# Optimization experiments

Measured on AMD Instinct MI355X. Metric: run time of the kernel, lower is better.

Reference implementation:

```python
import jax, jax.numpy as jnp
import numpy as np

EPS = 1e-6

def rms_norm(x):
    # RMSNorm, affine=False
    return x * jax.lax.rsqrt(jnp.mean(x * x, axis=-1, keepdims=True) + EPS)

def apply_rope(x, cos, sin):
    # x: [N, T, h, d], cos/sin: [T, d//2], half-split rotation
    x1, x2 = jnp.split(x, 2, axis=-1)
    c = cos[None, :, None, :]
    s = sin[None, :, None, :]
    return jnp.concatenate([x1 * c - x2 * s, x1 * s + x2 * c], axis=-1)

def setup_inputs() -> dict:
    key = jax.random.key(0)
    k0, k1, k2 = jax.random.split(key, 3)
    N, T, D, hd = 1, 2048, 2048, 128
    input_NTD = jax.random.normal(k0, (N, T, D), jnp.float32)
    qkv_weight = jax.random.normal(k1, (3, D, D), jnp.float32) / np.sqrt(D) / 2.0
    o_weight = jax.random.normal(k2, (D, D), jnp.float32) * 0.02
    # standard 1d RoPE angle table
    pos = jnp.arange(T, dtype=jnp.float32)
    inv_freq = 1.0 / (10000.0 ** (jnp.arange(hd // 2, dtype=jnp.float32) / (hd // 2)))
    ang = pos[:, None] * inv_freq[None, :]  # [T, hd//2]
    return {
        "input_NTD": input_NTD,
        "qkv_weight": qkv_weight,
        "o_weight": o_weight,
        "cos": jnp.cos(ang),
        "sin": jnp.sin(ang),
    }

def reference(input_NTD, qkv_weight, o_weight, cos, sin):
    N, T, D = input_NTD.shape
    hd = cos.shape[-1] * 2
    h = D // hd
    w = qkv_weight.reshape(3 * D, D)
    qkv = rms_norm(input_NTD) @ w.T                      # [N, T, 3D]
    qkv = qkv.reshape(N, T, 3 * h, hd)
    q, k, v = jnp.split(qkv, 3, axis=2)                  # each [N, T, h, hd]
    q = apply_rope(rms_norm(q), cos, sin)
    k = apply_rope(rms_norm(k), cos, sin)
    scale = 1.0 / np.sqrt(hd)
    scores = jnp.einsum('nqhd,nkhd->nhqk', q, k) * scale  # [N, h, T, T]
    causal = jnp.tril(jnp.ones((T, T), bool))
    scores = jnp.where(causal[None, None], scores, -jnp.inf)
    att = jax.nn.softmax(scores, axis=-1)
    x = jnp.einsum('nhqk,nkhd->nqhd', att, v).reshape(N, T, D)
    out = input_NTD + x @ o_weight.T
    return out, k, v
```

## Files before the change

kernel.cpp:

```cpp
#include <hip/hip_runtime.h>
#include <hip/hip_bf16.h>

typedef unsigned short u16;
typedef unsigned int u32;
typedef __bf16 bf16x8 __attribute__((ext_vector_type(8)));
typedef u16 u16x8 __attribute__((ext_vector_type(8)));
typedef u16 u16x4 __attribute__((ext_vector_type(4)));
typedef float f32x4 __attribute__((ext_vector_type(4)));

#define T_SEQ 2048
#define DMODEL 2048
#define NHEAD 16
#define HDIM 128
#define ATT_SCALE 0.08838834764831843f

__device__ __forceinline__ u16 f2bf(float f) {
    return __builtin_bit_cast(u16, __float2bfloat16(f));
}
__device__ __forceinline__ bf16x8 as_bf(u16x8 v) {
    return __builtin_bit_cast(bf16x8, v);
}
__device__ __forceinline__ float lo2f(u32 w) { return __builtin_bit_cast(float, w << 16); }
__device__ __forceinline__ float hi2f(u32 w) { return __builtin_bit_cast(float, w & 0xffff0000u); }
__device__ __forceinline__ void gload_lds16(const u16* g, u16* l) {
    __builtin_amdgcn_global_load_lds(
        (const __attribute__((address_space(1))) u32*)(g),
        (__attribute__((address_space(3))) u32*)(l), 16, 0, 0);
}

__global__ __launch_bounds__(256) void prep(const float* __restrict__ w1,
                                            const float* __restrict__ w2,
                                            const float* __restrict__ x,
                                            u16* __restrict__ d1,
                                            u16* __restrict__ d2,
                                            u16* __restrict__ xn) {
    const int b = blockIdx.x, tid = threadIdx.x;
    if (b < 8192) {
        int i = b * 256 + tid;
        const float* src; u16* dst; int k;
        if (i < 1572864) { src = w1; dst = d1; k = i; }
        else             { src = w2; dst = d2; k = i - 1572864; }
        float4 a = ((const float4*)src)[2 * k];
        float4 bb = ((const float4*)src)[2 * k + 1];
        u16x8 o;
        o[0] = f2bf(a.x); o[1] = f2bf(a.y); o[2] = f2bf(a.z); o[3] = f2bf(a.w);
        o[4] = f2bf(bb.x); o[5] = f2bf(bb.y); o[6] = f2bf(bb.z); o[7] = f2bf(bb.w);
        *(u16x8*)(dst + (size_t)k * 8) = o;
        return;
    }
    const int row = b - 8192;
    const float* xr = x + (size_t)row * DMODEL;
    float4 a = ((const float4*)xr)[2 * tid];
    float4 bb = ((const float4*)xr)[2 * tid + 1];
    float ss = a.x*a.x + a.y*a.y + a.z*a.z + a.w*a.w
             + bb.x*bb.x + bb.y*bb.y + bb.z*bb.z + bb.w*bb.w;
#pragma unroll
    for (int off = 32; off; off >>= 1) ss += __shfl_xor(ss, off);
    __shared__ float red[4];
    if ((tid & 63) == 0) red[tid >> 6] = ss;
    __syncthreads();
    float tot = red[0] + red[1] + red[2] + red[3];
    float r = rsqrtf(tot * (1.f / DMODEL) + 1e-6f);
    u16x8 o;
    o[0] = f2bf(a.x*r); o[1] = f2bf(a.y*r); o[2] = f2bf(a.z*r); o[3] = f2bf(a.w*r);
    o[4] = f2bf(bb.x*r); o[5] = f2bf(bb.y*r); o[6] = f2bf(bb.z*r); o[7] = f2bf(bb.w*r);
    *(u16x8*)(xn + (size_t)row * DMODEL + tid * 8) = o;
}

#define VM2 asm volatile("s_waitcnt vmcnt(2)" ::: "memory");
#define VM4 asm volatile("s_waitcnt vmcnt(4)" ::: "memory");
#define VM0 asm volatile("s_waitcnt vmcnt(0)" ::: "memory");

#define ENDP                                                                  \
  __builtin_amdgcn_s_barrier();                                               \
  __builtin_amdgcn_sched_barrier(0);

#define LDA192(BUF, MH)                                                       \
  _Pragma("unroll") for (int mq = 0; mq < 4; ++mq) {                          \
    int ra = wr + (MH) * 64 + mq * 16 + fr;                                   \
    int sw = ra & 7;                                                          \
    _Pragma("unroll") for (int k2 = 0; k2 < 2; ++k2)                          \
      av[mq][k2] = *(const u16x8*)(sA[BUF] + ra * 64 +                        \
                                   ((((k2 << 2) | fg) ^ sw) << 3));           \
  }

#define LDB0_192(BUF)                                                         \
  _Pragma("unroll") for (int nq = 0; nq < 2; ++nq) {                          \
    int rb = wc + nq * 16 + fr;                                               \
    int sw = rb & 7;                                                          \
    _Pragma("unroll") for (int k2 = 0; k2 < 2; ++k2)                          \
      bv[nq][k2] = *(const u16x8*)(sB[BUF] + rb * 64 +                        \
                                   ((((k2 << 2) | fg) ^ sw) << 3));           \
  }

#define LDB1_192(BUF)                                                         \
  {                                                                           \
    int rb = wc + 32 + fr;                                                    \
    int sw = rb & 7;                                                          \
    _Pragma("unroll") for (int k2 = 0; k2 < 2; ++k2)                          \
      bv1[k2] = *(const u16x8*)(sB[BUF] + rb * 64 +                           \
                                ((((k2 << 2) | fg) ^ sw) << 3));              \
  }

#define MFMAQ_N0(MH)                                                          \
  __builtin_amdgcn_s_barrier();                                               \
  __builtin_amdgcn_s_setprio(1);                                              \
  _Pragma("unroll") for (int k2 = 0; k2 < 2; ++k2)                            \
    _Pragma("unroll") for (int mq = 0; mq < 4; ++mq)                          \
      _Pragma("unroll") for (int nq = 0; nq < 2; ++nq)                        \
        acc[(MH) * 4 + mq][nq] = __builtin_amdgcn_mfma_f32_16x16x32_bf16(     \
            as_bf(av[mq][k2]), as_bf(bv[nq][k2]), acc[(MH) * 4 + mq][nq],     \
            0, 0, 0);                                                         \
  __builtin_amdgcn_s_setprio(0);

#define MFMAQ_N1(MH)                                                          \
  __builtin_amdgcn_s_barrier();                                               \
  __builtin_amdgcn_s_setprio(1);                                              \
  _Pragma("unroll") for (int k2 = 0; k2 < 2; ++k2)                            \
    _Pragma("unroll") for (int mq = 0; mq < 4; ++mq)                          \
      acc[(MH) * 4 + mq][2] = __builtin_amdgcn_mfma_f32_16x16x32_bf16(        \
          as_bf(av[mq][k2]), as_bf(bv1[k2]), acc[(MH) * 4 + mq][2],           \
          0, 0, 0);                                                           \
  __builtin_amdgcn_s_setprio(0);

__global__ __launch_bounds__(512) void gemm192(const u16* __restrict__ A,
                                               const u16* __restrict__ B,
                                               u16* __restrict__ C,
                                               int M, int N, int K) {
    extern __shared__ char smem[];
    const int tid = threadIdx.x, lane = tid & 63, wid = tid >> 6;
    const int bm = blockIdx.y * 256, bn = blockIdx.x * 192;
    const int wr = (wid >> 2) * 128, wc = (wid & 3) * 48;
    const int fr = lane & 15, fg = lane >> 4;

    u16* sA[2] = {(u16*)smem, (u16*)(smem + 57344)};
    u16* sB[2] = {(u16*)(smem + 32768), (u16*)(smem + 90112)};

    const int cs = (((tid & 7) ^ ((tid >> 3) & 7)) << 3);
    const int s8 = (tid & 7) << 3;
    const int rr6 = tid >> 3;

    auto stA = [&](int buf, int k0, int mh) {
#pragma unroll
        for (int j = 0; j < 2; ++j) {
            int r = j * 128 + mh * 64 + rr6;
            gload_lds16(A + (size_t)(bm + r) * K + k0 + cs, sA[buf] + r * 64 + s8);
        }
    };
    auto stB = [&](int buf, int k0, int bt) {
        int r = bt * 64 + rr6;
        gload_lds16(B + (size_t)(bn + r) * K + k0 + cs, sB[buf] + r * 64 + s8);
    };

    f32x4 acc[8][3] = {};
    u16x8 av[4][2], bv[2][2], bv1[2];
    const int nt = K >> 6;

    stA(0, 0, 0); stA(0, 0, 1); stB(0, 0, 0); stB(0, 0, 1); stB(0, 0, 2);
    stA(1, 64, 0);
    VM2
    __builtin_amdgcn_s_barrier();
    __builtin_amdgcn_sched_barrier(0);

    for (int it = 0; it < (nt >> 1); ++it) {
        const int kc = it << 7;
        const int kn1 = kc + 64, kn2 = kc + 128, kn3 = kc + 192;
        const bool st2 = (kn2 < K), st3 = (kn3 < K);

        LDA192(0, 0) LDB0_192(0)
        stA(1, kn1, 1); stB(1, kn1, 0);
        MFMAQ_N0(0) ENDP
        LDB1_192(0)
        stB(1, kn1, 1); stB(1, kn1, 2);
        MFMAQ_N1(0) ENDP
        LDA192(0, 1)
        if (st2) stA(0, kn2, 0);
        MFMAQ_N1(1) ENDP
        LDB0_192(0)
        MFMAQ_N0(1)
        if (st2) { VM2 } else { VM0 }
        ENDP
        LDA192(1, 0) LDB0_192(1)
        if (st2) { stA(0, kn2, 1); stB(0, kn2, 0); }
        MFMAQ_N0(0) ENDP
        LDB1_192(1)
        if (st2) { stB(0, kn2, 1); stB(0, kn2, 2); }
        MFMAQ_N1(0) ENDP
        LDA192(1, 1)
        if (st3) stA(1, kn3, 0);
        MFMAQ_N1(1) ENDP
        LDB0_192(1)
        MFMAQ_N0(1)
        if (st3) { VM2 } else { VM0 }
        ENDP
    }

#pragma unroll
    for (int am = 0; am < 8; ++am)
#pragma unroll
        for (int bq = 0; bq < 3; ++bq)
#pragma unroll
            for (int r = 0; r < 4; ++r) {
                int row = bm + wr + am * 16 + fg * 4 + r;
                int col = bn + wc + bq * 16 + fr;
                C[(size_t)row * N + col] = f2bf(acc[am][bq][r]);
            }
}

#define LDAH(BUF, MH)                                                         \
  _Pragma("unroll") for (int mq = 0; mq < 2; ++mq) {                          \
    int ra = wr + (MH) * 32 + mq * 16 + fr;                                   \
    int sw = ra & 7;                                                          \
    _Pragma("unroll") for (int k2 = 0; k2 < 2; ++k2)                          \
      av[mq][k2] = *(const u16x8*)(sA[BUF] + ra * 64 +                        \
                                   ((((k2 << 2) | fg) ^ sw) << 3));           \
  }

#define LDBH(BUF, NH)                                                         \
  _Pragma("unroll") for (int nq = 0; nq < 2; ++nq) {                          \
    int rb = wc + (NH) * 32 + nq * 16 + fr;                                   \
    int sw = rb & 7;                                                          \
    _Pragma("unroll") for (int k2 = 0; k2 < 2; ++k2)                          \
      bv[nq][k2] = *(const u16x8*)(sB[BUF] + rb * 64 +                        \
                                   ((((k2 << 2) | fg) ^ sw) << 3));           \
  }

#define MFMAQH(MH, NH)                                                        \
  __builtin_amdgcn_s_barrier();                                               \
  __builtin_amdgcn_s_setprio(1);                                              \
  _Pragma("unroll") for (int k2 = 0; k2 < 2; ++k2)                            \
    _Pragma("unroll") for (int mq = 0; mq < 2; ++mq)                          \
      _Pragma("unroll") for (int nq = 0; nq < 2; ++nq)                        \
        acc[(MH) * 2 + mq][(NH) * 2 + nq] =                                   \
            __builtin_amdgcn_mfma_f32_16x16x32_bf16(                          \
                as_bf(av[mq][k2]), as_bf(bv[nq][k2]),                         \
                acc[(MH) * 2 + mq][(NH) * 2 + nq], 0, 0, 0);                  \
  __builtin_amdgcn_s_setprio(0);

__global__ __launch_bounds__(256) void gemm128(const u16* __restrict__ A,
                                               const u16* __restrict__ B,
                                               float* __restrict__ C,
                                               const float* __restrict__ resid,
                                               int M, int N, int K) {
    extern __shared__ char smem[];
    const int tid = threadIdx.x, lane = tid & 63, wid = tid >> 6;
    const int bm = blockIdx.y * 128, bn = blockIdx.x * 128;
    const int wr = (wid >> 1) * 64, wc = (wid & 1) * 64;
    const int fr = lane & 15, fg = lane >> 4;

    u16* sA[2] = {(u16*)smem, (u16*)(smem + 32768)};
    u16* sB[2] = {(u16*)(smem + 16384), (u16*)(smem + 49152)};

    const int cs = (((tid & 7) ^ ((tid >> 3) & 7)) << 3);
    const int s8 = (tid & 7) << 3;
    const int rr5 = tid >> 3;

    auto stA = [&](int buf, int k0, int mh) {
#pragma unroll
        for (int j = 0; j < 2; ++j) {
            int r = j * 64 + mh * 32 + rr5;
            gload_lds16(A + (size_t)(bm + r) * K + k0 + cs, sA[buf] + r * 64 + s8);
        }
    };
    auto stB = [&](int buf, int k0, int nh) {
#pragma unroll
        for (int j = 0; j < 2; ++j) {
            int r = j * 64 + nh * 32 + rr5;
            gload_lds16(B + (size_t)(bn + r) * K + k0 + cs, sB[buf] + r * 64 + s8);
        }
    };

    f32x4 acc[4][4] = {};
    u16x8 av[2][2], bv[2][2];
    const int nt = K >> 6;

    stA(0, 0, 0); stA(0, 0, 1); stB(0, 0, 0); stB(0, 0, 1);
    stA(1, 64, 0); stB(1, 64, 1);
    VM4
    __builtin_amdgcn_s_barrier();
    __builtin_amdgcn_sched_barrier(0);

    for (int it = 0; it < (nt >> 1); ++it) {
        const int kc = it << 7;
        const int kn1 = kc + 64, kn2 = kc + 128, kn3 = kc + 192;
        const bool st2 = (kn2 < K), st3 = (kn3 < K);

        LDAH(0, 0) LDBH(0, 0)
        stA(1, kn1, 1);
        MFMAQH(0, 0) ENDP
        LDBH(0, 1)
        stB(1, kn1, 0);
        MFMAQH(0, 1) ENDP
        LDAH(0, 1)
        if (st2) stA(0, kn2, 0);
        MFMAQH(1, 1) ENDP
        LDBH(0, 0)
        if (st2) stB(0, kn2, 1);
        MFMAQH(1, 0)
        if (st2) { VM4 } else { VM0 }
        ENDP
        LDAH(1, 0) LDBH(1, 0)
        if (st2) stA(0, kn2, 1);
        MFMAQH(0, 0) ENDP
        LDBH(1, 1)
        if (st2) stB(0, kn2, 0);
        MFMAQH(0, 1) ENDP
        LDAH(1, 1)
        if (st3) stA(1, kn3, 0);
        MFMAQH(1, 1) ENDP
        LDBH(1, 0)
        if (st3) stB(1, kn3, 1);
        MFMAQH(1, 0)
        VM4
        ENDP
    }

#pragma unroll
    for (int am = 0; am < 4; ++am)
#pragma unroll
        for (int bq = 0; bq < 4; ++bq)
#pragma unroll
            for (int r = 0; r < 4; ++r) {
                int row = bm + wr + am * 16 + fg * 4 + r;
                int col = bn + wc + bq * 16 + fr;
                float val = acc[am][bq][r] + resid[(size_t)row * N + col];
                C[(size_t)row * N + col] = val;
            }
}

__global__ __launch_bounds__(256) void rope_split(const u16* __restrict__ qkv,
                                                  const float* __restrict__ cosb,
                                                  const float* __restrict__ sinb,
                                                  u16* __restrict__ q_bf,
                                                  u16* __restrict__ k_bf,
                                                  float* __restrict__ k_out,
                                                  float* __restrict__ v_out) {
    const int t = blockIdx.x, tid = threadIdx.x, wid = tid >> 6, lane = tid & 63;
    const u16* row = qkv + (size_t)t * (3 * DMODEL);
    const int dp = (lane & 31) << 1;
    float2 c2 = *(const float2*)(cosb + t * 64 + dp);
    float2 s2 = *(const float2*)(sinb + t * 64 + dp);
    const bool hi = lane >= 32;

    for (int task = wid; task < 32; task += 4) {
        u32 w = *(const u32*)(row + task * 128 + lane * 2);
        float xa = lo2f(w), xb = hi2f(w);
        float ss = xa * xa + xb * xb;
#pragma unroll
        for (int off = 32; off; off >>= 1) ss += __shfl_xor(ss, off);
        float rn = rsqrtf(ss * (1.f / 128.f) + 1e-6f);
        float pa = __shfl_xor(xa, 32), pb = __shfl_xor(xb, 32);
        float oa, ob;
        if (!hi) {
            oa = (xa * c2.x - pa * s2.x) * rn;
            ob = (xb * c2.y - pb * s2.y) * rn;
        } else {
            oa = (pa * s2.x + xa * c2.x) * rn;
            ob = (pb * s2.y + xb * c2.y) * rn;
        }
        u32 pk = (u32)f2bf(oa) | ((u32)f2bf(ob) << 16);
        if (task < 16) {
            *(u32*)(q_bf + ((size_t)task * T_SEQ + t) * 128 + lane * 2) = pk;
        } else {
            int hh = task - 16;
            *(u32*)(k_bf + ((size_t)hh * T_SEQ + t) * 128 + lane * 2) = pk;
            float2 kk; kk.x = oa; kk.y = ob;
            *(float2*)(k_out + (size_t)t * DMODEL + hh * 128 + lane * 2) = kk;
        }
    }
    {
        u16x8 vv = *(const u16x8*)(row + 2 * DMODEL + tid * 8);
        float4 f0, f1;
        f0.x = __builtin_bit_cast(float, (u32)vv[0] << 16);
        f0.y = __builtin_bit_cast(float, (u32)vv[1] << 16);
        f0.z = __builtin_bit_cast(float, (u32)vv[2] << 16);
        f0.w = __builtin_bit_cast(float, (u32)vv[3] << 16);
        f1.x = __builtin_bit_cast(float, (u32)vv[4] << 16);
        f1.y = __builtin_bit_cast(float, (u32)vv[5] << 16);
        f1.z = __builtin_bit_cast(float, (u32)vv[6] << 16);
        f1.w = __builtin_bit_cast(float, (u32)vv[7] << 16);
        *(float4*)(v_out + (size_t)t * DMODEL + tid * 8) = f0;
        *(float4*)(v_out + (size_t)t * DMODEL + tid * 8 + 4) = f1;
    }
}

__global__ __launch_bounds__(256) void vtrans(const u16* __restrict__ qkv,
                                              u16* __restrict__ vt) {
    const int b = blockIdx.x, tid = threadIdx.x;
    const int head = b >> 7;
    const int i = (b & 127) * 256 + tid;
    const int d = i & 127, tc = i >> 7;
    u16x8 o;
#pragma unroll
    for (int j = 0; j < 8; ++j)
        o[j] = qkv[(size_t)(tc * 8 + j) * (3 * DMODEL) + 2 * DMODEL + head * 128 + d];
    *(u16x8*)&vt[((size_t)head * 128 + d) * T_SEQ + tc * 8] = o;
}

__global__ __launch_bounds__(256) void attn_fwd(const u16* __restrict__ qb,
                                                const u16* __restrict__ kb,
                                                const u16* __restrict__ vtb,
                                                u16* __restrict__ xout) {
    __shared__ u16 Ks[2][64 * 128];
    __shared__ u16 Vs[2][128 * 64];
    __shared__ u16 Ps[4][16 * 64];

    const int bid = blockIdx.x;
    const int r8 = bid & 7, s = bid >> 3;
    const int head = r8 + ((s >> 5) << 3);
    const int j = s & 31;
    const int qt = (s < 32) ? (31 - j) : j;

    const int tid = threadIdx.x, wid = tid >> 6, lane = tid & 63;
    const int fr = lane & 15, fg = lane >> 4;
    const u16* kh = kb + (size_t)head * T_SEQ * 128;
    const u16* vth = vtb + (size_t)head * 128 * T_SEQ;
    const u16* qh = qb + (size_t)head * T_SEQ * 128;
    const int q0 = qt * 64 + wid * 16;
    const int qrow_g = q0 + fr;

    u16x8 bq[4];
    {
        const u16* qrow = qh + (size_t)(q0 + fr) * 128 + fg * 8;
#pragma unroll
        for (int cc = 0; cc < 4; ++cc) bq[cc] = *(const u16x8*)(qrow + cc * 32);
    }

    auto stage = [&](int kv0, int buf) {
#pragma unroll
        for (int i = 0; i < 4; ++i) {
            int idx = i * 256 + tid;
            int r = idx >> 4;
            int cbs = ((idx & 15) << 4) ^ ((r & 7) << 4);
            gload_lds16(kh + (size_t)(kv0 + r) * 128 + (cbs >> 1), &Ks[buf][idx * 8]);
        }
#pragma unroll
        for (int i = 0; i < 4; ++i) {
            int idx = i * 256 + tid;
            int d = idx >> 3;
            int cbs = ((idx & 7) << 4) ^ ((d & 7) << 4);
            gload_lds16(vth + (size_t)d * T_SEQ + kv0 + (cbs >> 1), &Vs[buf][idx * 8]);
        }
    };

    stage(0, 0);

    f32x4 o[8] = {};
    float m_run = -1e30f, l_run = 0.f;
    const int nt = qt + 1;

    for (int kt = 0; kt < nt; ++kt) {
        const int kv0 = kt * 64;
        const int buf = kt & 1;
        if (kt + 1 < nt) {
            stage(kv0 + 64, buf ^ 1);
            asm volatile("s_waitcnt vmcnt(8)" ::: "memory");
        } else {
            asm volatile("s_waitcnt vmcnt(0)" ::: "memory");
        }
        __builtin_amdgcn_s_barrier();
        __builtin_amdgcn_sched_barrier(0);

        const char* ksb = (const char*)&Ks[buf][0];
        const char* vsb = (const char*)&Vs[buf][0];
        char* psb = (char*)&Ps[wid][0];

        float p[4][4];
        float mx = -1e30f;
        const bool diag = (kv0 + 64 > q0);
#pragma unroll
        for (int st = 0; st < 4; ++st) {
            f32x4 sacc = {0.f, 0.f, 0.f, 0.f};
#pragma unroll
            for (int c4 = 0; c4 < 4; ++c4) {
                int r = st * 16 + fr;
                int cb = c4 * 64 + fg * 16;
                u16x8 ak = *(const u16x8*)(ksb + r * 256 + (cb ^ ((r & 7) << 4)));
                sacc = __builtin_amdgcn_mfma_f32_16x16x32_bf16(
                    as_bf(ak), as_bf(bq[c4]), sacc, 0, 0, 0);
            }
#pragma unroll
            for (int rr = 0; rr < 4; ++rr) {
                float sv = sacc[rr] * ATT_SCALE;
                if (diag) {
                    int kvg = kv0 + st * 16 + fg * 4 + rr;
                    sv = (kvg <= qrow_g) ? sv : -1e30f;
                }
                p[st][rr] = sv;
                mx = fmaxf(mx, sv);
            }
        }
        mx = fmaxf(mx, __shfl_xor(mx, 16));
        mx = fmaxf(mx, __shfl_xor(mx, 32));

        if (__all(mx - m_run <= 8.f)) {
            float rs = 0.f;
#pragma unroll
            for (int st = 0; st < 4; ++st) {
                u16x4 pw;
#pragma unroll
                for (int rr = 0; rr < 4; ++rr) {
                    float e = __expf(p[st][rr] - m_run);
                    rs += e;
                    pw[rr] = f2bf(e);
                }
                *(u16x4*)(psb + fr * 128 + ((st * 32 + fg * 8) ^ ((fr & 7) << 4))) = pw;
            }
            rs += __shfl_xor(rs, 16);
            rs += __shfl_xor(rs, 32);
            l_run += rs;
        } else {
            float m_new = fmaxf(m_run, mx);
            float corr = __expf(m_run - m_new);
            float rs = 0.f;
#pragma unroll
            for (int st = 0; st < 4; ++st) {
                u16x4 pw;
#pragma unroll
                for (int rr = 0; rr < 4; ++rr) {
                    float e = __expf(p[st][rr] - m_new);
                    rs += e;
                    pw[rr] = f2bf(e);
                }
                *(u16x4*)(psb + fr * 128 + ((st * 32 + fg * 8) ^ ((fr & 7) << 4))) = pw;
            }
            rs += __shfl_xor(rs, 16);
            rs += __shfl_xor(rs, 32);
            l_run = l_run * corr + rs;
            m_run = m_new;
            float ct[4];
#pragma unroll
            for (int rr = 0; rr < 4; ++rr) ct[rr] = __shfl(corr, fg * 4 + rr);
#pragma unroll
            for (int f = 0; f < 8; ++f)
#pragma unroll
                for (int rr = 0; rr < 4; ++rr) o[f][rr] *= ct[rr];
        }

#pragma unroll
        for (int ks = 0; ks < 2; ++ks) {
            u16x8 pa = *(const u16x8*)(psb + fr * 128 + ((ks * 64 + fg * 16) ^ ((fr & 7) << 4)));
#pragma unroll
            for (int f = 0; f < 8; ++f) {
                int d = f * 16 + fr;
                u16x8 vB = *(const u16x8*)(vsb + d * 128 + ((ks * 64 + fg * 16) ^ ((d & 7) << 4)));
                o[f] = __builtin_amdgcn_mfma_f32_16x16x32_bf16(
                    as_bf(pa), as_bf(vB), o[f], 0, 0, 0);
            }
        }
        __builtin_amdgcn_s_barrier();
    }

    float li[4];
#pragma unroll
    for (int rr = 0; rr < 4; ++rr) li[rr] = __shfl(l_run, fg * 4 + rr);
#pragma unroll
    for (int f = 0; f < 8; ++f)
#pragma unroll
        for (int rr = 0; rr < 4; ++rr) {
            int trow = q0 + fg * 4 + rr;
            float val = o[f][rr] / li[rr];
            xout[(size_t)trow * DMODEL + head * 128 + f * 16 + fr] = f2bf(val);
        }
}

extern "C" void kernel_launch(void* const* d_in, const int* in_sizes, int n_in,
                              void* d_out, int out_size, void* d_ws, size_t ws_size,
                              hipStream_t stream) {
    const float* x_in = (const float*)d_in[0];
    const float* w_qkv = (const float*)d_in[1];
    const float* w_o = (const float*)d_in[2];
    const float* cosb = (const float*)d_in[3];
    const float* sinb = (const float*)d_in[4];

    float* out = (float*)d_out;
    float* k_out = out + 4194304;
    float* v_out = out + 8388608;

    char* ws = (char*)d_ws;
    u16* xn    = (u16*)(ws);
    u16* w_bf  = (u16*)(ws + (size_t)(8u << 20));
    u16* o_bf  = (u16*)(ws + (size_t)(32u << 20));
    u16* qkv   = (u16*)(ws + (size_t)(40u << 20));
    u16* q_bf  = (u16*)(ws + (size_t)(64u << 20));
    u16* k_bf  = (u16*)(ws + (size_t)(72u << 20));
    u16* vt_bf = (u16*)(ws + (size_t)(80u << 20));
    u16* x_bf  = (u16*)(ws + (size_t)(88u << 20));

    (void)hipFuncSetAttribute(reinterpret_cast<const void*>(&gemm192),
                              hipFuncAttributeMaxDynamicSharedMemorySize, 114688);
    (void)hipFuncSetAttribute(reinterpret_cast<const void*>(&gemm128),
                              hipFuncAttributeMaxDynamicSharedMemorySize, 65536);

    prep<<<10240, 256, 0, stream>>>(w_qkv, w_o, x_in, w_bf, o_bf, xn);
    gemm192<<<dim3(32, 8), 512, 114688, stream>>>(xn, w_bf, qkv, 2048, 6144, 2048);
    rope_split<<<2048, 256, 0, stream>>>(qkv, cosb, sinb, q_bf, k_bf, k_out, v_out);
    vtrans<<<2048, 256, 0, stream>>>(qkv, vt_bf);
    attn_fwd<<<512, 256, 0, stream>>>(q_bf, k_bf, vt_bf, x_bf);
    gemm128<<<dim3(16, 16), 256, 65536, stream>>>(x_bf, o_bf, out, x_in, 2048, 2048, 2048);
}
```

Before: 179.3 us.

## Split causal attention KV range across two blocks and merge partial results

Attention is split so each (head, query tile) is processed by two blocks covering halves of the KV tiles. Each block writes an unnormalized bf16 partial output plus running max and sum, and a new merge kernel combines them. The aim is more parallel blocks and better load balance on the GPU. In exchange, the K/V double buffering is removed (each tile is loaded and waited on synchronously), and an extra kernel launch and partial-result memory traffic are added.

```diff
diff --git a/kernel.cpp b/kernel.cpp
--- a/kernel.cpp
+++ b/kernel.cpp
@@ -22,6 +22,7 @@
 }
 __device__ __forceinline__ float lo2f(u32 w) { return __builtin_bit_cast(float, w << 16); }
 __device__ __forceinline__ float hi2f(u32 w) { return __builtin_bit_cast(float, w & 0xffff0000u); }
+__device__ __forceinline__ float bf2f(u16 v) { return __builtin_bit_cast(float, (u32)v << 16); }
 __device__ __forceinline__ void gload_lds16(const u16* g, u16* l) {
     __builtin_amdgcn_global_load_lds(
         (const __attribute__((address_space(1))) u32*)(g),
@@ -371,14 +372,8 @@
     {
         u16x8 vv = *(const u16x8*)(row + 2 * DMODEL + tid * 8);
         float4 f0, f1;
-        f0.x = __builtin_bit_cast(float, (u32)vv[0] << 16);
-        f0.y = __builtin_bit_cast(float, (u32)vv[1] << 16);
-        f0.z = __builtin_bit_cast(float, (u32)vv[2] << 16);
-        f0.w = __builtin_bit_cast(float, (u32)vv[3] << 16);
-        f1.x = __builtin_bit_cast(float, (u32)vv[4] << 16);
-        f1.y = __builtin_bit_cast(float, (u32)vv[5] << 16);
-        f1.z = __builtin_bit_cast(float, (u32)vv[6] << 16);
-        f1.w = __builtin_bit_cast(float, (u32)vv[7] << 16);
+        f0.x = bf2f(vv[0]); f0.y = bf2f(vv[1]); f0.z = bf2f(vv[2]); f0.w = bf2f(vv[3]);
+        f1.x = bf2f(vv[4]); f1.y = bf2f(vv[5]); f1.z = bf2f(vv[6]); f1.w = bf2f(vv[7]);
         *(float4*)(v_out + (size_t)t * DMODEL + tid * 8) = f0;
         *(float4*)(v_out + (size_t)t * DMODEL + tid * 8 + 4) = f1;
     }
@@ -397,19 +392,25 @@
     *(u16x8*)&vt[((size_t)head * 128 + d) * T_SEQ + tc * 8] = o;
 }
 
-__global__ __launch_bounds__(256) void attn_fwd(const u16* __restrict__ qb,
-                                                const u16* __restrict__ kb,
-                                                const u16* __restrict__ vtb,
-                                                u16* __restrict__ xout) {
-    __shared__ u16 Ks[2][64 * 128];
-    __shared__ u16 Vs[2][128 * 64];
+__global__ __launch_bounds__(256) void attn_part(const u16* __restrict__ qb,
+                                                 const u16* __restrict__ kb,
+                                                 const u16* __restrict__ vtb,
+                                                 u16* __restrict__ opart,
+                                                 float* __restrict__ ml) {
+    __shared__ u16 Ks[64 * 128];
+    __shared__ u16 Vs[128 * 64];
     __shared__ u16 Ps[4][16 * 64];
 
     const int bid = blockIdx.x;
     const int r8 = bid & 7, s = bid >> 3;
-    const int head = r8 + ((s >> 5) << 3);
-    const int j = s & 31;
-    const int qt = (s < 32) ? (31 - j) : j;
+    const int hs = s >> 6, g = (s >> 5) & 1, m = s & 31;
+    const int head = r8 + (hs << 3);
+    const int qt = g ? (31 - m) : m;
+    const int nt = qt + 1;
+    const int h0c = (nt + 1) >> 1;
+    const int first = g ? h0c : 0;
+    const int count = g ? (nt - h0c) : h0c;
+    const int pidx = (head * 32 + qt) * 2 + g;
 
     const int tid = threadIdx.x, wid = tid >> 6, lane = tid & 63;
     const int fr = lane & 15, fg = lane >> 4;
@@ -426,43 +427,35 @@
         for (int cc = 0; cc < 4; ++cc) bq[cc] = *(const u16x8*)(qrow + cc * 32);
     }
 
-    auto stage = [&](int kv0, int buf) {
+    auto stage = [&](int kv0) {
 #pragma unroll
         for (int i = 0; i < 4; ++i) {
             int idx = i * 256 + tid;
             int r = idx >> 4;
             int cbs = ((idx & 15) << 4) ^ ((r & 7) << 4);
-            gload_lds16(kh + (size_t)(kv0 + r) * 128 + (cbs >> 1), &Ks[buf][idx * 8]);
+            gload_lds16(kh + (size_t)(kv0 + r) * 128 + (cbs >> 1), &Ks[idx * 8]);
         }
 #pragma unroll
         for (int i = 0; i < 4; ++i) {
             int idx = i * 256 + tid;
             int d = idx >> 3;
             int cbs = ((idx & 7) << 4) ^ ((d & 7) << 4);
-            gload_lds16(vth + (size_t)d * T_SEQ + kv0 + (cbs >> 1), &Vs[buf][idx * 8]);
+            gload_lds16(vth + (size_t)d * T_SEQ + kv0 + (cbs >> 1), &Vs[idx * 8]);
         }
     };
-
-    stage(0, 0);
 
     f32x4 o[8] = {};
     float m_run = -1e30f, l_run = 0.f;
-    const int nt = qt + 1;
-
-    for (int kt = 0; kt < nt; ++kt) {
-        const int kv0 = kt * 64;
-        const int buf = kt & 1;
-        if (kt + 1 < nt) {
-            stage(kv0 + 64, buf ^ 1);
-            asm volatile("s_waitcnt vmcnt(8)" ::: "memory");
-        } else {
-            asm volatile("s_waitcnt vmcnt(0)" ::: "memory");
-        }
+
+    for (int i = 0; i < count; ++i) {
+        const int kv0 = (first + i) * 64;
+        stage(kv0);
+        asm volatile("s_waitcnt vmcnt(0)" ::: "memory");
         __builtin_amdgcn_s_barrier();
         __builtin_amdgcn_sched_barrier(0);
 
-        const char* ksb = (const char*)&Ks[buf][0];
-        const char* vsb = (const char*)&Vs[buf][0];
+        const char* ksb = (const char*)&Ks[0];
+        const char* vsb = (const char*)&Vs[0];
         char* psb = (char*)&Ps[wid][0];
 
         float p[4][4];
@@ -549,19 +542,49 @@
             }
         }
         __builtin_amdgcn_s_barrier();
-    }
-
-    float li[4];
-#pragma unroll
-    for (int rr = 0; rr < 4; ++rr) li[rr] = __shfl(l_run, fg * 4 + rr);
+        __builtin_amdgcn_sched_barrier(0);
+    }
+
+    u16* op = opart + (size_t)pidx * 8192;
 #pragma unroll
     for (int f = 0; f < 8; ++f)
 #pragma unroll
-        for (int rr = 0; rr < 4; ++rr) {
-            int trow = q0 + fg * 4 + rr;
-            float val = o[f][rr] / li[rr];
-            xout[(size_t)trow * DMODEL + head * 128 + f * 16 + fr] = f2bf(val);
-        }
+        for (int rr = 0; rr < 4; ++rr)
+            op[(wid * 16 + fg * 4 + rr) * 128 + f * 16 + fr] = f2bf(o[f][rr]);
+    if (fg == 0) {
+        ml[pidx * 128 + wid * 16 + fr] = m_run;
+        ml[pidx * 128 + 64 + wid * 16 + fr] = l_run;
+    }
+}
+
+__global__ __launch_bounds__(256) void attn_merge(const u16* __restrict__ opart,
+                                                  const float* __restrict__ ml,
+                                                  u16* __restrict__ xout) {
+    const int b = blockIdx.x, tid = threadIdx.x;
+    const int head = b >> 5, qt = b & 31;
+    const int p0 = b * 2, p1 = b * 2 + 1;
+    const int row = tid >> 2, d0 = (tid & 3) * 32;
+
+    float m0 = ml[p0 * 128 + row], l0 = ml[p0 * 128 + 64 + row];
+    float m1 = ml[p1 * 128 + row], l1 = ml[p1 * 128 + 64 + row];
+    float M = fmaxf(m0, m1);
+    float w0 = __expf(m0 - M), w1 = __expf(m1 - M);
+    float inv = 1.f / (l0 * w0 + l1 * w1);
+    w0 *= inv; w1 *= inv;
+
+    const u16* a0 = opart + (size_t)p0 * 8192 + row * 128 + d0;
+    const u16* a1 = opart + (size_t)p1 * 8192 + row * 128 + d0;
+    u16* dst = xout + (size_t)(qt * 64 + row) * DMODEL + head * 128 + d0;
+#pragma unroll
+    for (int j = 0; j < 4; ++j) {
+        u16x8 v0 = *(const u16x8*)(a0 + j * 8);
+        u16x8 v1 = *(const u16x8*)(a1 + j * 8);
+        u16x8 ov;
+#pragma unroll
+        for (int e = 0; e < 8; ++e)
+            ov[e] = f2bf(bf2f(v0[e]) * w0 + bf2f(v1[e]) * w1);
+        *(u16x8*)(dst + j * 8) = ov;
+    }
 }
 
 extern "C" void kernel_launch(void* const* d_in, const int* in_sizes, int n_in,
@@ -586,6 +609,8 @@
     u16* k_bf  = (u16*)(ws + (size_t)(72u << 20));
     u16* vt_bf = (u16*)(ws + (size_t)(80u << 20));
     u16* x_bf  = (u16*)(ws + (size_t)(88u << 20));
+    u16* opart = (u16*)(ws + (size_t)(40u << 20));
+    float* mlb = (float*)(ws + (size_t)(56u << 20));
 
     (void)hipFuncSetAttribute(reinterpret_cast<const void*>(&gemm192),
                               hipFuncAttributeMaxDynamicSharedMemorySize, 114688);
@@ -596,6 +621,7 @@
     gemm192<<<dim3(32, 8), 512, 114688, stream>>>(xn, w_bf, qkv, 2048, 6144, 2048);
     rope_split<<<2048, 256, 0, stream>>>(qkv, cosb, sinb, q_bf, k_bf, k_out, v_out);
     vtrans<<<2048, 256, 0, stream>>>(qkv, vt_bf);
-    attn_fwd<<<512, 256, 0, stream>>>(q_bf, k_bf, vt_bf, x_bf);
+    attn_part<<<1024, 256, 0, stream>>>(q_bf, k_bf, vt_bf, opart, mlb);
+    attn_merge<<<512, 256, 0, stream>>>(opart, mlb, x_bf);
     gemm128<<<dim3(16, 16), 256, 65536, stream>>>(x_bf, o_bf, out, x_in, 2048, 2048, 2048);
 }
```

After: 177.0 us. No clear change (-1.3%).
